# Performance work log

Hardware: AMD Instinct MI355X
Metric: run time of the kernel (lower is better)

The kernel has to match this reference:

```python
import jax, jax.numpy as jnp
import numpy as np

NUM_HEADS = 12
EPS = 1e-5


def _pool_norm(t, w, g, b, thw, stride):
    # t: [B, heads, 1+L, hd]. Depthwise Conv3d pooling on non-cls tokens, then LayerNorm(hd).
    B, Hn, _, hd = t.shape
    cls, body = t[:, :, :1], t[:, :, 1:]
    T, Hs, Ws = thw
    x = body.reshape(B * Hn, T, Hs, Ws, hd).transpose(0, 4, 1, 2, 3)  # [B*heads, hd, T, H, W]
    pad = [(w.shape[2] // 2,) * 2, (w.shape[3] // 2,) * 2, (w.shape[4] // 2,) * 2]
    y = jax.lax.conv_general_dilated(x, w, window_strides=stride, padding=pad,
                                     feature_group_count=hd,
                                     dimension_numbers=('NCDHW', 'OIDHW', 'NCDHW'))
    Tp, Hp, Wp = y.shape[2], y.shape[3], y.shape[4]
    y = y.reshape(B, Hn, hd, Tp * Hp * Wp).transpose(0, 1, 3, 2)  # [B, heads, Lp, hd]
    y = jnp.concatenate([cls, y], axis=2)
    mu = y.mean(-1, keepdims=True)
    var = ((y - mu) ** 2).mean(-1, keepdims=True)
    return (y - mu) * jax.lax.rsqrt(var + EPS) * g + b


def _forward(x, Wq, Wk, Wv, Wproj, b_proj, pq, pk, pv, gq, bq, gk, bk, gv, bv, thw):
    B, N, C = x.shape
    hd = C // NUM_HEADS
    def proj(W):
        return (x @ W.T).reshape(B, N, NUM_HEADS, hd).transpose(0, 2, 1, 3)  # [B, heads, N, hd]
    q = _pool_norm(proj(Wq), pq, gq, bq, thw, (1, 2, 2))
    k = _pool_norm(proj(Wk), pk, gk, bk, thw, (1, 4, 4))
    v = _pool_norm(proj(Wv), pv, gv, bv, thw, (1, 4, 4))
    scale = hd ** -0.5
    attn = jax.nn.softmax(jnp.einsum('bhqd,bhkd->bhqk', q * scale, k), axis=-1)
    o = jnp.einsum('bhqk,bhkd->bhqd', attn, v)
    o = o.transpose(0, 2, 1, 3).reshape(B, o.shape[2], C)
    return o @ Wproj.T + b_proj


def setup_inputs() -> dict:
    key = jax.random.key(0)
    ks = jax.random.split(key, 8)
    B, T, H, W, C = 8, 8, 28, 28, 768
    hd = C // NUM_HEADS
    N = T * H * W + 1  # cls token
    s = lambda k, sh: jax.random.normal(k, sh, jnp.float32) * 0.02
    return {
        'x': jax.random.normal(ks[0], (B, N, C), jnp.float32),
        'Wq': s(ks[1], (C, C)), 'Wk': s(ks[2], (C, C)), 'Wv': s(ks[3], (C, C)),
        'Wproj': s(ks[4], (C, C)), 'b_proj': jnp.zeros((C,), jnp.float32),
        'pool_q_w': s(ks[5], (hd, 1, 3, 3, 3)),
        'pool_k_w': s(ks[6], (hd, 1, 3, 3, 3)),
        'pool_v_w': s(ks[7], (hd, 1, 3, 3, 3)),
        'gq': jnp.ones((hd,), jnp.float32), 'bq': jnp.zeros((hd,), jnp.float32),
        'gk': jnp.ones((hd,), jnp.float32), 'bk': jnp.zeros((hd,), jnp.float32),
        'gv': jnp.ones((hd,), jnp.float32), 'bv': jnp.zeros((hd,), jnp.float32),
        'thw_t': 8, 'thw_h': 28, 'thw_w': 28,
    }


def reference(x, Wq, Wk, Wv, Wproj, b_proj, pool_q_w, pool_k_w, pool_v_w,
              gq, bq, gk, bk, gv, bv, thw_t, thw_h, thw_w):
    return _forward(x, Wq, Wk, Wv, Wproj, b_proj, pool_q_w, pool_k_w, pool_v_w,
                    gq, bq, gk, bk, gv, bv, (thw_t, thw_h, thw_w))
```

## Files before the change

kernel.cpp:

```cpp
#include <hip/hip_runtime.h>

using bf16   = __bf16;
using bf16x4 = __attribute__((ext_vector_type(4))) __bf16;
using bf16x8 = __attribute__((ext_vector_type(8))) __bf16;
using f32x4  = __attribute__((ext_vector_type(4))) float;
using u32x4  = __attribute__((ext_vector_type(4))) unsigned int;

#define MFMA16(a,b,c) __builtin_amdgcn_mfma_f32_16x16x32_bf16((a),(b),(c),0,0,0)

__device__ inline void glds16(const void* g, void* l) {
    __builtin_amdgcn_global_load_lds(
        (__attribute__((address_space(1))) void*)(const_cast<void*>(g)),
        (__attribute__((address_space(3))) void*)(l), 16, 0, 0);
}

__device__ inline int xcd_remap(int bid, int nwg) {
    const int xcd = bid & 7, loc = bid >> 3;
    const int q8 = nwg >> 3, r8 = nwg & 7;
    return (xcd < r8 ? xcd * (q8 + 1) : r8 * (q8 + 1) + (xcd - r8) * q8) + loc;
}

constexpr int CB   = 8;
constexpr int NH   = 12;
constexpr int CC   = 768;
constexpr int HD   = 64;
constexpr int TT   = 8, HH = 28, WW = 28;
constexpr int NTOK = TT*HH*WW + 1;
constexpr int MX   = CB*NTOK;
constexpr int MXP  = 50304;
constexpr int NQ   = 1569, NQP = 1600;
constexpr int NK   = 393,  NKP = 416;
constexpr int MO   = CB*NQ;
constexpr int MOP  = 12672;
constexpr int CTOK = 1 + TT*20*20;
constexpr int MKV  = CB*CTOK;
constexpr int MKVP = 25856;

__global__ __launch_bounds__(256) void cast_f32_bf16(const float* __restrict__ src,
                                                     bf16* __restrict__ dst,
                                                     int nvalid, int ntotal) {
    int i = (blockIdx.x * 256 + threadIdx.x) * 4;
    int stride = gridDim.x * 256 * 4;
    for (; i < ntotal; i += stride) {
        bf16x4 o;
        if (i + 3 < nvalid) {
            f32x4 v = *(const f32x4*)(src + i);
            #pragma unroll
            for (int e = 0; e < 4; ++e) o[e] = (bf16)v[e];
        } else {
            #pragma unroll
            for (int e = 0; e < 4; ++e) {
                int k = i + e;
                o[e] = (bf16)((k < nvalid) ? src[k] : 0.f);
            }
        }
        *(bf16x4*)(dst + i) = o;
    }
}

__global__ __launch_bounds__(256) void cast_w4(const float* __restrict__ w0,
                                               const float* __restrict__ w1,
                                               const float* __restrict__ w2,
                                               const float* __restrict__ w3,
                                               bf16* __restrict__ dst) {
    constexpr int WSZ = 589824;
    int i = (blockIdx.x * 256 + threadIdx.x) * 4;
    if (i >= 4 * WSZ) return;
    const int setn = i / WSZ, j = i % WSZ;
    const float* src = (setn == 0) ? w0 : (setn == 1) ? w1 : (setn == 2) ? w2 : w3;
    f32x4 v = *(const f32x4*)(src + j);
    bf16x4 o;
    #pragma unroll
    for (int e = 0; e < 4; ++e) o[e] = (bf16)v[e];
    *(bf16x4*)(dst + i) = o;
}

__global__ __launch_bounds__(256) void transpose_w3(const float* __restrict__ w0,
                                                    const float* __restrict__ w1,
                                                    const float* __restrict__ w2,
                                                    float* __restrict__ wt) {
    int i = blockIdx.x * 256 + threadIdx.x;
    if (i >= 3 * 1728) return;
    int setn = i / 1728, j = i % 1728;
    const float* src = (setn == 0) ? w0 : (setn == 1) ? w1 : w2;
    int tap = j / 64, c = j % 64;
    wt[i] = src[c * 27 + tap];
}

__global__ void bound_kernel(const float* __restrict__ gq, const float* __restrict__ bq,
                             const float* __restrict__ gk, const float* __restrict__ bk,
                             float* __restrict__ out) {
    const int c = threadIdx.x;
    float mgq = fabsf(gq[c]), sbq = bq[c] * bq[c];
    float mgk = fabsf(gk[c]), sbk = bk[c] * bk[c];
    #pragma unroll
    for (int m = 1; m < 64; m <<= 1) {
        mgq = fmaxf(mgq, __shfl_xor(mgq, m)); sbq += __shfl_xor(sbq, m);
        mgk = fmaxf(mgk, __shfl_xor(mgk, m)); sbk += __shfl_xor(sbk, m);
    }
    if (c == 0) {
        const float Bq = 8.f * mgq + sqrtf(sbq);
        const float Bk = 8.f * mgk + sqrtf(sbk);
        out[0] = 0.125f * Bq * Bk;
    }
}

__global__ __launch_bounds__(512, 2) void gemmU(const bf16* __restrict__ xb,
                                                const bf16* __restrict__ wqkv,
                                                bf16* __restrict__ tmpq,
                                                bf16* __restrict__ tmpkv) {
    extern __shared__ char lds[];
    const int wgid = xcd_remap(blockIdx.x, gridDim.x);

    const int tid = threadIdx.x, lane = tid & 63, w = tid >> 6;
    const int li = lane & 15, lg = lane >> 4;
    const int wr = w >> 2, wc = w & 3;
    const int lr  = lane >> 3;
    const int lsw = ((lane & 7) ^ lr) << 3;

    const bool isQ = wgid < 591;
    int bm, bn, Mv, ldc;
    const bf16* Bb;
    bf16* C;
    if (isQ) { bm = wgid / 3;        bn = wgid % 3;        Mv = MXP;  ldc = 768;
               Bb = wqkv + (size_t)bn * 256 * 768;               C = tmpq; }
    else     { int t = wgid - 591;   bm = t / 6; bn = t % 6; Mv = MKVP; ldc = 1536;
               Bb = wqkv + (size_t)(768 + bn * 256) * 768;       C = tmpkv; }

    const bf16* abase[4];
    const bf16* bbase[4];
    #pragma unroll
    for (int h_ = 0; h_ < 4; ++h_) {
        int gr = bm * 256 + h_ * 64 + w * 8 + lr;
        size_t orig;
        if (isQ) {
            if (gr > MXP - 1) gr = MXP - 1;
            orig = (size_t)gr;
        } else {
            if (gr > MKV - 1) gr = MKV - 1;
            const unsigned b = (unsigned)gr / 3201u;
            const unsigned p = (unsigned)gr % 3201u;
            if (p == 0) orig = (size_t)b * NTOK;
            else {
                const unsigned q  = p - 1;
                const unsigned t2 = q / 400u, rem = q % 400u;
                const unsigned hi = rem / 20u, wi = rem % 20u;
                const int ih = 4 * (int)((hi + 1) / 3) + (int)((hi + 1) % 3) - 1;
                const int iw = 4 * (int)((wi + 1) / 3) + (int)((wi + 1) % 3) - 1;
                orig = (size_t)b * NTOK + 1 + ((size_t)t2 * HH + ih) * WW + iw;
            }
        }
        abase[h_] = xb + orig * 768 + lsw;
        bbase[h_] = Bb + (size_t)(h_ * 64 + w * 8 + lr) * 768 + lsw;
    }

    const int sw_  = (li & 7) << 4;
    const int swc0 = (lg * 16) ^ sw_;
    const int swc1 = (64 | (lg * 16)) ^ sw_;

#define STAGE_AH(Tt, a) do {                                                         \
        char* d_ = lds + ((Tt) & 1) * 65536;                                         \
        glds16(abase[2*(a)]   + (size_t)(Tt) * 64, d_ + ((2*(a))   * 64 + w * 8) * 128); \
        glds16(abase[2*(a)+1] + (size_t)(Tt) * 64, d_ + ((2*(a)+1) * 64 + w * 8) * 128); \
    } while (0)
#define STAGE_BH(Tt, b) do {                                                         \
        char* d_ = lds + ((Tt) & 1) * 65536 + 32768;                                 \
        glds16(bbase[2*(b)]   + (size_t)(Tt) * 64, d_ + ((2*(b))   * 64 + w * 8) * 128); \
        glds16(bbase[2*(b)+1] + (size_t)(Tt) * 64, d_ + ((2*(b)+1) * 64 + w * 8) * 128); \
    } while (0)

    f32x4 acc[8][4] = {};
    bf16x8 aF[4][2], bF0[2][2], bF1[2][2];

#define READ_A(mh)                                                                   \
    _Pragma("unroll") for (int mf = 0; mf < 4; ++mf) {                               \
        const char* p_ = bufA + (size_t)(wr * 128 + (mh) * 64 + mf * 16 + li) * 128; \
        aF[mf][0] = *(const bf16x8*)(p_ + swc0);                                     \
        aF[mf][1] = *(const bf16x8*)(p_ + swc1); }
#define READ_B(nh, BF)                                                               \
    _Pragma("unroll") for (int nf = 0; nf < 2; ++nf) {                               \
        const char* p_ = bufB + (size_t)(wc * 64 + (nh) * 32 + nf * 16 + li) * 128;  \
        BF[nf][0] = *(const bf16x8*)(p_ + swc0);                                     \
        BF[nf][1] = *(const bf16x8*)(p_ + swc1); }
#define MFMA_PH(mh, nh, BF)                                                          \
    _Pragma("unroll") for (int mf = 0; mf < 4; ++mf)                                 \
    _Pragma("unroll") for (int nf = 0; nf < 2; ++nf) {                               \
        acc[(mh)*4+mf][(nh)*2+nf] = MFMA16(aF[mf][0], BF[nf][0], acc[(mh)*4+mf][(nh)*2+nf]); \
        acc[(mh)*4+mf][(nh)*2+nf] = MFMA16(aF[mf][1], BF[nf][1], acc[(mh)*4+mf][(nh)*2+nf]); }

    STAGE_BH(0, 0); STAGE_BH(0, 1); STAGE_AH(0, 0); STAGE_AH(0, 1);
    STAGE_BH(1, 0); STAGE_BH(1, 1); STAGE_AH(1, 0);
    asm volatile("s_waitcnt vmcnt(6)" ::: "memory");
    __builtin_amdgcn_s_barrier();

    #pragma unroll
    for (int k = 0; k < 12; ++k) {
        const char* bufA = lds + (k & 1) * 65536;
        const char* bufB = bufA + 32768;
        READ_A(0); READ_B(0, bF0);
        if (k < 11) STAGE_AH(k + 1, 1);
        __builtin_amdgcn_s_barrier();
        asm volatile("s_waitcnt lgkmcnt(0)" ::: "memory");
        __builtin_amdgcn_s_setprio(1);
        MFMA_PH(0, 0, bF0);
        __builtin_amdgcn_s_setprio(0);
        __builtin_amdgcn_s_barrier();
        READ_B(1, bF1);
        __builtin_amdgcn_s_barrier();
        asm volatile("s_waitcnt lgkmcnt(0)" ::: "memory");
        __builtin_amdgcn_s_setprio(1);
        MFMA_PH(0, 1, bF1);
        __builtin_amdgcn_s_setprio(0);
        __builtin_amdgcn_s_barrier();
        READ_A(1);
        if (k < 10) { STAGE_BH(k + 2, 0); STAGE_BH(k + 2, 1); }
        __builtin_amdgcn_s_barrier();
        asm volatile("s_waitcnt lgkmcnt(0)" ::: "memory");
        __builtin_amdgcn_s_setprio(1);
        MFMA_PH(1, 0, bF0);
        __builtin_amdgcn_s_setprio(0);
        __builtin_amdgcn_s_barrier();
        if (k < 10) STAGE_AH(k + 2, 0);
        __builtin_amdgcn_s_barrier();
        __builtin_amdgcn_s_setprio(1);
        MFMA_PH(1, 1, bF1);
        __builtin_amdgcn_s_setprio(0);
        if (k < 10)       asm volatile("s_waitcnt vmcnt(6)" ::: "memory");
        else if (k == 10) asm volatile("s_waitcnt vmcnt(0)" ::: "memory");
        __builtin_amdgcn_s_barrier();
    }
#undef STAGE_AH
#undef STAGE_BH
#undef READ_A
#undef READ_B
#undef MFMA_PH

    #pragma unroll
    for (int mf = 0; mf < 8; ++mf) {
        const int row0 = bm * 256 + wr * 128 + mf * 16 + lg * 4;
        #pragma unroll
        for (int nf = 0; nf < 4; ++nf) {
            const int col = bn * 256 + wc * 64 + nf * 16 + li;
            #pragma unroll
            for (int r = 0; r < 4; ++r) {
                const int row = row0 + r;
                if (row < Mv)
                    C[(size_t)row * ldc + col] = (bf16)acc[mf][nf][r];
            }
        }
    }
}

__global__ __launch_bounds__(512, 2) void gemmF(const bf16* __restrict__ A,
                                                const bf16* __restrict__ Bw,
                                                float* __restrict__ Cptr,
                                                const float* __restrict__ bias,
                                                int nbn, int Mvalid, int Aclamp) {
    extern __shared__ char lds[];
    const int wgid = xcd_remap(blockIdx.x, gridDim.x);
    const int bm = wgid / nbn, bn = wgid % nbn;

    const int tid = threadIdx.x, lane = tid & 63, w = tid >> 6;
    const int li = lane & 15, lg = lane >> 4;
    const int wr = w >> 2, wc = w & 3;
    const int lr  = lane >> 3;
    const int lsw = ((lane & 7) ^ lr) << 3;
    const bf16* Agp = A  + (size_t)bm * 256 * 768;
    const bf16* Bgp = Bw + (size_t)bn * 128 * 768;
    const int clampA = Aclamp - bm * 256;

    const int sw_  = (li & 7) << 4;
    const int swc0 = (lg * 16) ^ sw_;
    const int swc1 = (64 | (lg * 16)) ^ sw_;

#define STAGE_T(Tt, buf) do {                                                        \
        char* d_ = lds + (buf) * 49152;                                              \
        _Pragma("unroll")                                                            \
        for (int h_ = 0; h_ < 4; ++h_) {                                             \
            const int r0_ = h_ * 64 + w * 8;                                         \
            int gr_ = r0_ + lr; if (gr_ >= clampA) gr_ = clampA - 1;                 \
            glds16(Agp + (size_t)gr_ * 768 + (Tt) * 64 + lsw, d_ + r0_ * 128);       \
        }                                                                            \
        _Pragma("unroll")                                                            \
        for (int h_ = 0; h_ < 2; ++h_) {                                             \
            const int r0_ = h_ * 64 + w * 8;                                         \
            glds16(Bgp + (size_t)(r0_ + lr) * 768 + (Tt) * 64 + lsw,                 \
                   d_ + 32768 + r0_ * 128);                                          \
        } } while (0)

    f32x4 acc[8][2] = {};
    bf16x8 aF[8], bF[2];

#define READ_K(sw)                                                                   \
    _Pragma("unroll") for (int mf = 0; mf < 8; ++mf)                                 \
        aF[mf] = *(const bf16x8*)(bufA + (size_t)(wr * 128 + mf * 16 + li) * 128 + (sw)); \
    _Pragma("unroll") for (int nf = 0; nf < 2; ++nf)                                 \
        bF[nf] = *(const bf16x8*)(bufB + (size_t)(wc * 32 + nf * 16 + li) * 128 + (sw));

#define MFMA_K()                                                                     \
    _Pragma("unroll") for (int mf = 0; mf < 8; ++mf)                                 \
    _Pragma("unroll") for (int nf = 0; nf < 2; ++nf)                                 \
        acc[mf][nf] = MFMA16(aF[mf], bF[nf], acc[mf][nf]);

    STAGE_T(0, 0);
    STAGE_T(1, 1);
    asm volatile("s_waitcnt vmcnt(6)" ::: "memory");
    __builtin_amdgcn_s_barrier();
    __builtin_amdgcn_sched_barrier(0);

    #pragma unroll
    for (int T = 0; T < 12; ++T) {
        const char* bufA = lds + (T & 1) * 49152;
        const char* bufB = bufA + 32768;
        if (T >= 1 && T < 11) STAGE_T(T + 1, (T + 1) & 1);
        READ_K(swc0);
        __builtin_amdgcn_s_setprio(1);
        MFMA_K();
        __builtin_amdgcn_s_setprio(0);
        READ_K(swc1);
        __builtin_amdgcn_s_setprio(1);
        MFMA_K();
        __builtin_amdgcn_s_setprio(0);
        asm volatile("s_waitcnt lgkmcnt(0)" ::: "memory");
        if (T < 11) asm volatile("s_waitcnt vmcnt(0)" ::: "memory");
        __builtin_amdgcn_s_barrier();
        __builtin_amdgcn_sched_barrier(0);
    }
#undef STAGE_T
#undef READ_K
#undef MFMA_K

    #pragma unroll
    for (int mf = 0; mf < 8; ++mf) {
        const int row0 = bm * 256 + wr * 128 + mf * 16 + lg * 4;
        #pragma unroll
        for (int nf = 0; nf < 2; ++nf) {
            const int col = bn * 128 + wc * 32 + nf * 16 + li;
            #pragma unroll
            for (int r = 0; r < 4; ++r) {
                const int row = row0 + r;
                if (row < Mvalid)
                    Cptr[(size_t)row * 768 + col] = acc[mf][nf][r] + bias[col];
            }
        }
    }
}

template<int S, int OH, int OW, int CH, int NP, int NPpad, int SRCSTRIDE, bool COMPACT>
__global__ __launch_bounds__(256) void pool_norm2(const bf16* __restrict__ P,
                                                  const float* __restrict__ wt,
                                                  const float* __restrict__ gamma,
                                                  const float* __restrict__ beta,
                                                  bf16* __restrict__ outp,
                                                  float outScale) {
    constexpr int TASKS = TT * OH * CH + 1;
    const int w = threadIdx.x >> 6, lane = threadIdx.x & 63;
    const int gw = xcd_remap(blockIdx.x, gridDim.x) * 4 + w;
    const int bh = gw / TASKS, task = gw % TASKS;
    const int b = bh / NH, head = bh % NH;
    const int owg = lane >> 3, cg = lane & 7, c = cg * 8;
    const size_t rowbase = COMPACT ? (size_t)b * CTOK : (size_t)b * NTOK;
    const size_t pbase = rowbase * SRCSTRIDE + head * HD + c;

    if (task == TASKS - 1) {
        if (owg == 0) {
            bf16x8 v = *(const bf16x8*)(P + pbase);
            float a[8];
            #pragma unroll
            for (int e = 0; e < 8; ++e) a[e] = (float)v[e];
            float s = 0;
            #pragma unroll
            for (int e = 0; e < 8; ++e) s += a[e];
            s += __shfl_xor(s, 1); s += __shfl_xor(s, 2); s += __shfl_xor(s, 4);
            const float mu = s * 0.015625f;
            float v2 = 0;
            #pragma unroll
            for (int e = 0; e < 8; ++e) { float d = a[e] - mu; v2 += d * d; }
            v2 += __shfl_xor(v2, 1); v2 += __shfl_xor(v2, 2); v2 += __shfl_xor(v2, 4);
            const float rs = rsqrtf(v2 * 0.015625f + 1e-5f);
            f32x4 g0 = *(const f32x4*)(gamma + c), g1 = *(const f32x4*)(gamma + c + 4);
            f32x4 b0 = *(const f32x4*)(beta + c),  b1 = *(const f32x4*)(beta + c + 4);
            bf16x8 o;
            #pragma unroll
            for (int e = 0; e < 4; ++e) {
                o[e]     = (bf16)(((a[e]     - mu) * rs * g0[e] + b0[e]) * outScale);
                o[4 + e] = (bf16)(((a[4 + e] - mu) * rs * g1[e] + b1[e]) * outScale);
            }
            *(bf16x8*)(outp + ((size_t)bh * NPpad) * HD + c) = o;
        } else {
            bf16x8 z = {};
            for (int p = NP + owg - 1; p < NPpad; p += 7)
                *(bf16x8*)(outp + ((size_t)bh * NPpad + p) * HD + c) = z;
        }
        return;
    }

    const int t  = task / (OH * CH);
    const int r2 = task % (OH * CH);
    const int oh = r2 / CH;
    const int ow = (r2 % CH) * 8 + owg;
    const bool active = (ow < OW);

    float acc[8] = {0, 0, 0, 0, 0, 0, 0, 0};
    #pragma unroll
    for (int dt = 0; dt < 3; ++dt) {
        const int it = t + dt - 1;
        if (it < 0 || it >= TT) continue;
        #pragma unroll
        for (int dh = 0; dh < 3; ++dh) {
            int rowh;
            if constexpr (COMPACT) {
                const int hi = 3 * oh + dh - 1;
                if (hi < 0) continue;
                rowh = 1 + it * 400 + hi * 20;
            } else {
                const int ih = oh * S + dh - 1;
                if (ih < 0 || ih >= HH) continue;
                rowh = 1 + (it * HH + ih) * WW;
            }
            #pragma unroll
            for (int dw = 0; dw < 3; ++dw) {
                int rowoff;
                bool ok;
                if constexpr (COMPACT) {
                    const int wi = 3 * ow + dw - 1;
                    ok = active && (wi >= 0);
                    rowoff = rowh + wi;
                } else {
                    const int iw = ow * S + dw - 1;
                    ok = active && (iw >= 0);
                    rowoff = rowh + iw;
                }
                if (ok) {
                    bf16x8 v = *(const bf16x8*)(P + pbase + (size_t)rowoff * SRCSTRIDE);
                    const float* wp = wt + ((dt * 3 + dh) * 3 + dw) * 64 + c;
                    f32x4 w0 = *(const f32x4*)wp, w1 = *(const f32x4*)(wp + 4);
                    #pragma unroll
                    for (int e = 0; e < 4; ++e) {
                        acc[e]     += w0[e] * (float)v[e];
                        acc[4 + e] += w1[e] * (float)v[4 + e];
                    }
                }
            }
        }
    }
    float s = 0;
    #pragma unroll
    for (int e = 0; e < 8; ++e) s += acc[e];
    s += __shfl_xor(s, 1); s += __shfl_xor(s, 2); s += __shfl_xor(s, 4);
    const float mu = s * 0.015625f;
    float v2 = 0;
    #pragma unroll
    for (int e = 0; e < 8; ++e) { float d = acc[e] - mu; v2 += d * d; }
    v2 += __shfl_xor(v2, 1); v2 += __shfl_xor(v2, 2); v2 += __shfl_xor(v2, 4);
    const float rs = rsqrtf(v2 * 0.015625f + 1e-5f);
    if (active) {
        f32x4 g0 = *(const f32x4*)(gamma + c), g1 = *(const f32x4*)(gamma + c + 4);
        f32x4 b0 = *(const f32x4*)(beta + c),  b1 = *(const f32x4*)(beta + c + 4);
        bf16x8 o;
        #pragma unroll
        for (int e = 0; e < 4; ++e) {
            o[e]     = (bf16)(((acc[e]     - mu) * rs * g0[e] + b0[e]) * outScale);
            o[4 + e] = (bf16)(((acc[4 + e] - mu) * rs * g1[e] + b1[e]) * outScale);
        }
        const int p = 1 + (t * OH + oh) * OW + ow;
        *(bf16x8*)(outp + ((size_t)bh * NPpad + p) * HD + c) = o;
    }
}

__global__ __launch_bounds__(256) void attn_kernel(const bf16* __restrict__ qn,
                                                   const bf16* __restrict__ kn,
                                                   const bf16* __restrict__ vn,
                                                   bf16* __restrict__ ob,
                                                   const float* __restrict__ Mptr) {
    __shared__ bf16 Kl[2][32][72];
    __shared__ bf16 Vt[2][64][40];
    __shared__ bf16 Pl[4][16][40];

    const int tid = threadIdx.x, l = tid & 63, w = tid >> 6;
    const int li = l & 15, lg = l >> 4;
    const int wgid = xcd_remap(blockIdx.x, gridDim.x);
    const int bh = wgid / 25;
    const int b = bh / NH, head = bh % NH;
    const int qbase = (wgid % 25) * 64 + w * 16;
    const float M = Mptr[0];

    const bf16* qp = qn + ((size_t)bh * NQP + qbase + li) * HD + lg * 8;
    const bf16x8 aq0 = *(const bf16x8*)qp;
    const bf16x8 aq1 = *(const bf16x8*)(qp + 32);

    const int srow = tid >> 3, scol = (tid & 7) * 8;
    const int sj = tid & 31, sd8 = tid >> 5;
    const bf16* kbase = kn + (size_t)bh * NKP * HD;
    const bf16* vbase = vn + (size_t)bh * NKP * HD;

    u32x4 kv = *(const u32x4*)(kbase + srow * HD + scol);
    u32x4 vv = *(const u32x4*)(vbase + sj * HD + sd8 * 8);
    *(u32x4*)&Kl[0][srow][scol] = kv;
    {
        bf16x8 t = __builtin_bit_cast(bf16x8, vv);
        #pragma unroll
        for (int e = 0; e < 8; ++e) Vt[0][sd8 * 8 + e][sj] = t[e];
    }

    f32x4 oacc[4] = {};
    float lpart[4] = {0.f, 0.f, 0.f, 0.f};

    for (int kt = 0; kt < 13; ++kt) {
        const int cur = kt & 1;
        if (kt < 12) {
            kv = *(const u32x4*)(kbase + (kt + 1) * 32 * HD + srow * HD + scol);
            vv = *(const u32x4*)(vbase + (kt + 1) * 32 * HD + sj * HD + sd8 * 8);
        }
        __syncthreads();

        f32x4 c0 = {}, c1 = {};
        const bf16x8 b00 = *(const bf16x8*)&Kl[cur][li][lg * 8];
        const bf16x8 b01 = *(const bf16x8*)&Kl[cur][li][32 + lg * 8];
        const bf16x8 b10 = *(const bf16x8*)&Kl[cur][16 + li][lg * 8];
        const bf16x8 b11 = *(const bf16x8*)&Kl[cur][16 + li][32 + lg * 8];
        __builtin_amdgcn_s_setprio(1);
        c0 = MFMA16(aq0, b00, c0); c0 = MFMA16(aq1, b01, c0);
        c1 = MFMA16(aq0, b10, c1); c1 = MFMA16(aq1, b11, c1);
        __builtin_amdgcn_s_setprio(0);

        float p0[4], p1[4];
        #pragma unroll
        for (int r = 0; r < 4; ++r) {
            p0[r] = __expf(c0[r] - M);
            p1[r] = __expf(c1[r] - M);
        }
        if (kt == 12) {
            const bool m0 = (384 + li) >= NK;
            #pragma unroll
            for (int r = 0; r < 4; ++r) { if (m0) p0[r] = 0.f; p1[r] = 0.f; }
        }
        #pragma unroll
        for (int r = 0; r < 4; ++r) {
            lpart[r] += p0[r] + p1[r];
            Pl[w][lg * 4 + r][li]      = (bf16)p0[r];
            Pl[w][lg * 4 + r][16 + li] = (bf16)p1[r];
        }
        const bf16x8 ap = *(const bf16x8*)&Pl[w][li][lg * 8];
        __builtin_amdgcn_s_setprio(1);
        #pragma unroll
        for (int dg = 0; dg < 4; ++dg) {
            const bf16x8 bv = *(const bf16x8*)&Vt[cur][dg * 16 + li][lg * 8];
            oacc[dg] = MFMA16(ap, bv, oacc[dg]);
        }
        __builtin_amdgcn_s_setprio(0);

        if (kt < 12) {
            const int nxt = cur ^ 1;
            *(u32x4*)&Kl[nxt][srow][scol] = kv;
            bf16x8 t = __builtin_bit_cast(bf16x8, vv);
            #pragma unroll
            for (int e = 0; e < 8; ++e) Vt[nxt][sd8 * 8 + e][sj] = t[e];
        }
    }
    #pragma unroll
    for (int r = 0; r < 4; ++r) {
        float lsum = lpart[r];
        lsum += __shfl_xor(lsum, 1);
        lsum += __shfl_xor(lsum, 2);
        lsum += __shfl_xor(lsum, 4);
        lsum += __shfl_xor(lsum, 8);
        const int q = qbase + lg * 4 + r;
        if (q < NQ) {
            const float inv = 1.f / lsum;
            const size_t off = ((size_t)(b * NQ + q)) * CC + head * HD;
            #pragma unroll
            for (int dg = 0; dg < 4; ++dg)
                ob[off + dg * 16 + li] = (bf16)(oacc[dg][r] * inv);
        }
    }
}

extern "C" void kernel_launch(void* const* d_in, const int* in_sizes, int n_in,
                              void* d_out, int out_size, void* d_ws, size_t ws_size,
                              hipStream_t stream) {
    const float* x     = (const float*)d_in[0];
    const float* Wq    = (const float*)d_in[1];
    const float* Wk    = (const float*)d_in[2];
    const float* Wv    = (const float*)d_in[3];
    const float* Wproj = (const float*)d_in[4];
    const float* bproj = (const float*)d_in[5];
    const float* pqw   = (const float*)d_in[6];
    const float* pkw   = (const float*)d_in[7];
    const float* pvw   = (const float*)d_in[8];
    const float* gq    = (const float*)d_in[9];
    const float* bq    = (const float*)d_in[10];
    const float* gk    = (const float*)d_in[11];
    const float* bk    = (const float*)d_in[12];
    const float* gv    = (const float*)d_in[13];
    const float* bv    = (const float*)d_in[14];

    if (ws_size < 364000000ULL) return;
    char* ws = (char*)d_ws;
    bf16* xb    = (bf16*)(ws);
    bf16* wqkv  = (bf16*)(ws + 77266944);
    bf16* wpb   = (bf16*)(ws + 80805888);
    bf16* tmpq  = (bf16*)(ws + 81985536);
    bf16* tmpkv = (bf16*)(ws + 159252480);
    bf16* qn    = (bf16*)(ws + 238682112);
    bf16* kn    = (bf16*)(ws + 258342912);
    bf16* vnb   = (bf16*)(ws + 263454720);
    bf16* ob    = (bf16*)(ws + 268566528);
    float* wt   = (float*)(ws + 288030720);
    float* Mb   = (float*)(ws + 288051456);

    (void)hipFuncSetAttribute((const void*)gemmU,
                              hipFuncAttributeMaxDynamicSharedMemorySize, 131072);
    (void)hipFuncSetAttribute((const void*)gemmF,
                              hipFuncAttributeMaxDynamicSharedMemorySize, 98304);

    transpose_w3<<<21, 256, 0, stream>>>(pqw, pkw, pvw, wt);
    bound_kernel<<<1, 64, 0, stream>>>(gq, bq, gk, bk, Mb);
    cast_f32_bf16<<<4096, 256, 0, stream>>>(x, xb, MX * CC, MXP * CC);
    cast_w4<<<2304, 256, 0, stream>>>(Wq, Wk, Wv, Wproj, wqkv);

    gemmU<<<1197, 512, 131072, stream>>>(xb, wqkv, tmpq, tmpkv);

    pool_norm2<2, 14, 14, 2, NQ, NQP, 768,  false><<<5400, 256, 0, stream>>>(tmpq,        wt,        gq, bq, qn,  0.125f);
    pool_norm2<4, 7, 7, 1, NK, NKP, 1536, true ><<<1368, 256, 0, stream>>>(tmpkv,       wt + 1728, gk, bk, kn,  1.0f);
    pool_norm2<4, 7, 7, 1, NK, NKP, 1536, true ><<<1368, 256, 0, stream>>>(tmpkv + 768, wt + 3456, gv, bv, vnb, 1.0f);

    attn_kernel<<<2400, 256, 0, stream>>>(qn, kn, vnb, ob, Mb);

    gemmF<<<50 * 6, 512, 98304, stream>>>(ob, wpb, (float*)d_out, bproj, 6, MO, MOP);
}
```

Baseline: 349.6 us.

## Stage Q pooling input slabs in LDS and merge prep and KV pooling launches

The three small prep kernels (weight cast, pool-weight transpose, bound computation) become one launch. Q pooling now runs per (batch, output row, head) block. Each block stages the needed input rows for all time steps in LDS, so overlapping conv taps read shared memory instead of global memory. K and V pooling, plus the Q cls-token and padding work, are merged into one kernel, which cuts launch count. The cost is about 100KB of LDS per Q block, which limits occupancy, and a larger LDS staging phase behind a barrier.

```diff
diff --git a/kernel.cpp b/kernel.cpp
--- a/kernel.cpp
+++ b/kernel.cpp
@@ -58,50 +58,47 @@
     }
 }
 
-__global__ __launch_bounds__(256) void cast_w4(const float* __restrict__ w0,
-                                               const float* __restrict__ w1,
-                                               const float* __restrict__ w2,
-                                               const float* __restrict__ w3,
-                                               bf16* __restrict__ dst) {
+__global__ __launch_bounds__(256) void prep(const float* __restrict__ Wq, const float* __restrict__ Wk,
+                                            const float* __restrict__ Wv, const float* __restrict__ Wp,
+                                            const float* __restrict__ pqw, const float* __restrict__ pkw,
+                                            const float* __restrict__ pvw,
+                                            const float* __restrict__ gq, const float* __restrict__ bq,
+                                            const float* __restrict__ gk, const float* __restrict__ bk,
+                                            bf16* __restrict__ wdst, float* __restrict__ wt,
+                                            float* __restrict__ Mb) {
     constexpr int WSZ = 589824;
-    int i = (blockIdx.x * 256 + threadIdx.x) * 4;
-    if (i >= 4 * WSZ) return;
-    const int setn = i / WSZ, j = i % WSZ;
-    const float* src = (setn == 0) ? w0 : (setn == 1) ? w1 : (setn == 2) ? w2 : w3;
-    f32x4 v = *(const f32x4*)(src + j);
-    bf16x4 o;
-    #pragma unroll
-    for (int e = 0; e < 4; ++e) o[e] = (bf16)v[e];
-    *(bf16x4*)(dst + i) = o;
-}
-
-__global__ __launch_bounds__(256) void transpose_w3(const float* __restrict__ w0,
-                                                    const float* __restrict__ w1,
-                                                    const float* __restrict__ w2,
-                                                    float* __restrict__ wt) {
-    int i = blockIdx.x * 256 + threadIdx.x;
-    if (i >= 3 * 1728) return;
-    int setn = i / 1728, j = i % 1728;
-    const float* src = (setn == 0) ? w0 : (setn == 1) ? w1 : w2;
-    int tap = j / 64, c = j % 64;
-    wt[i] = src[c * 27 + tap];
-}
-
-__global__ void bound_kernel(const float* __restrict__ gq, const float* __restrict__ bq,
-                             const float* __restrict__ gk, const float* __restrict__ bk,
-                             float* __restrict__ out) {
-    const int c = threadIdx.x;
-    float mgq = fabsf(gq[c]), sbq = bq[c] * bq[c];
-    float mgk = fabsf(gk[c]), sbk = bk[c] * bk[c];
-    #pragma unroll
-    for (int m = 1; m < 64; m <<= 1) {
-        mgq = fmaxf(mgq, __shfl_xor(mgq, m)); sbq += __shfl_xor(sbq, m);
-        mgk = fmaxf(mgk, __shfl_xor(mgk, m)); sbk += __shfl_xor(sbk, m);
-    }
-    if (c == 0) {
-        const float Bq = 8.f * mgq + sqrtf(sbq);
-        const float Bk = 8.f * mgk + sqrtf(sbk);
-        out[0] = 0.125f * Bq * Bk;
+    const int bid = blockIdx.x, tid = threadIdx.x;
+    if (bid < 2304) {
+        int i = (bid * 256 + tid) * 4;
+        const int setn = i / WSZ, j = i % WSZ;
+        const float* src = (setn == 0) ? Wq : (setn == 1) ? Wk : (setn == 2) ? Wv : Wp;
+        f32x4 v = *(const f32x4*)(src + j);
+        bf16x4 o;
+        #pragma unroll
+        for (int e = 0; e < 4; ++e) o[e] = (bf16)v[e];
+        *(bf16x4*)(wdst + i) = o;
+    } else if (bid < 2325) {
+        int i = (bid - 2304) * 256 + tid;
+        if (i < 3 * 1728) {
+            int setn = i / 1728, j = i % 1728;
+            const float* src = (setn == 0) ? pqw : (setn == 1) ? pkw : pvw;
+            int tap = j / 64, c = j % 64;
+            wt[i] = src[c * 27 + tap];
+        }
+    } else if (tid < 64) {
+        const int c = tid;
+        float mgq = fabsf(gq[c]), sbq = bq[c] * bq[c];
+        float mgk = fabsf(gk[c]), sbk = bk[c] * bk[c];
+        #pragma unroll
+        for (int m = 1; m < 64; m <<= 1) {
+            mgq = fmaxf(mgq, __shfl_xor(mgq, m)); sbq += __shfl_xor(sbq, m);
+            mgk = fmaxf(mgk, __shfl_xor(mgk, m)); sbk += __shfl_xor(sbk, m);
+        }
+        if (c == 0) {
+            const float Bq = 8.f * mgq + sqrtf(sbq);
+            const float Bk = 8.f * mgk + sqrtf(sbk);
+            Mb[0] = 0.125f * Bq * Bk;
+        }
     }
 }
 
@@ -346,94 +343,62 @@
     }
 }
 
-template<int S, int OH, int OW, int CH, int NP, int NPpad, int SRCSTRIDE, bool COMPACT>
-__global__ __launch_bounds__(256) void pool_norm2(const bf16* __restrict__ P,
-                                                  const float* __restrict__ wt,
-                                                  const float* __restrict__ gamma,
-                                                  const float* __restrict__ beta,
-                                                  bf16* __restrict__ outp,
-                                                  float outScale) {
-    constexpr int TASKS = TT * OH * CH + 1;
-    const int w = threadIdx.x >> 6, lane = threadIdx.x & 63;
-    const int gw = xcd_remap(blockIdx.x, gridDim.x) * 4 + w;
-    const int bh = gw / TASKS, task = gw % TASKS;
-    const int b = bh / NH, head = bh % NH;
-    const int owg = lane >> 3, cg = lane & 7, c = cg * 8;
-    const size_t rowbase = COMPACT ? (size_t)b * CTOK : (size_t)b * NTOK;
-    const size_t pbase = rowbase * SRCSTRIDE + head * HD + c;
-
-    if (task == TASKS - 1) {
-        if (owg == 0) {
-            bf16x8 v = *(const bf16x8*)(P + pbase);
-            float a[8];
-            #pragma unroll
-            for (int e = 0; e < 8; ++e) a[e] = (float)v[e];
-            float s = 0;
-            #pragma unroll
-            for (int e = 0; e < 8; ++e) s += a[e];
-            s += __shfl_xor(s, 1); s += __shfl_xor(s, 2); s += __shfl_xor(s, 4);
-            const float mu = s * 0.015625f;
-            float v2 = 0;
-            #pragma unroll
-            for (int e = 0; e < 8; ++e) { float d = a[e] - mu; v2 += d * d; }
-            v2 += __shfl_xor(v2, 1); v2 += __shfl_xor(v2, 2); v2 += __shfl_xor(v2, 4);
-            const float rs = rsqrtf(v2 * 0.015625f + 1e-5f);
-            f32x4 g0 = *(const f32x4*)(gamma + c), g1 = *(const f32x4*)(gamma + c + 4);
-            f32x4 b0 = *(const f32x4*)(beta + c),  b1 = *(const f32x4*)(beta + c + 4);
-            bf16x8 o;
-            #pragma unroll
-            for (int e = 0; e < 4; ++e) {
-                o[e]     = (bf16)(((a[e]     - mu) * rs * g0[e] + b0[e]) * outScale);
-                o[4 + e] = (bf16)(((a[4 + e] - mu) * rs * g1[e] + b1[e]) * outScale);
-            }
-            *(bf16x8*)(outp + ((size_t)bh * NPpad) * HD + c) = o;
-        } else {
-            bf16x8 z = {};
-            for (int p = NP + owg - 1; p < NPpad; p += 7)
-                *(bf16x8*)(outp + ((size_t)bh * NPpad + p) * HD + c) = z;
-        }
-        return;
-    }
-
-    const int t  = task / (OH * CH);
-    const int r2 = task % (OH * CH);
-    const int oh = r2 / CH;
-    const int ow = (r2 % CH) * 8 + owg;
-    const bool active = (ow < OW);
-
-    float acc[8] = {0, 0, 0, 0, 0, 0, 0, 0};
-    #pragma unroll
-    for (int dt = 0; dt < 3; ++dt) {
-        const int it = t + dt - 1;
-        if (it < 0 || it >= TT) continue;
-        #pragma unroll
-        for (int dh = 0; dh < 3; ++dh) {
-            int rowh;
-            if constexpr (COMPACT) {
-                const int hi = 3 * oh + dh - 1;
-                if (hi < 0) continue;
-                rowh = 1 + it * 400 + hi * 20;
-            } else {
-                const int ih = oh * S + dh - 1;
-                if (ih < 0 || ih >= HH) continue;
-                rowh = 1 + (it * HH + ih) * WW;
-            }
-            #pragma unroll
-            for (int dw = 0; dw < 3; ++dw) {
-                int rowoff;
-                bool ok;
-                if constexpr (COMPACT) {
-                    const int wi = 3 * ow + dw - 1;
-                    ok = active && (wi >= 0);
-                    rowoff = rowh + wi;
-                } else {
-                    const int iw = ow * S + dw - 1;
-                    ok = active && (iw >= 0);
-                    rowoff = rowh + iw;
-                }
-                if (ok) {
-                    bf16x8 v = *(const bf16x8*)(P + pbase + (size_t)rowoff * SRCSTRIDE);
-                    const float* wp = wt + ((dt * 3 + dh) * 3 + dw) * 64 + c;
+__global__ __launch_bounds__(256) void pool_q_slab(const bf16* __restrict__ tmpq,
+                                                   const float* __restrict__ wt,
+                                                   const float* __restrict__ gamma,
+                                                   const float* __restrict__ beta,
+                                                   bf16* __restrict__ qn) {
+    extern __shared__ char smem[];
+    bf16*  slab = (bf16*)smem;
+    float* wl   = (float*)(smem + 96768);
+    const int bid = blockIdx.x;
+    const int head = bid % 12;
+    int r = bid / 12;
+    const int oh = r % 14;
+    const int b  = r / 14;
+    const int tid = threadIdx.x;
+
+    for (int i = tid; i < 27 * 64; i += 256) wl[i] = wt[i];
+
+    const size_t gbase = ((size_t)b * NTOK + 1) * 768 + head * 64;
+    #pragma unroll
+    for (int dh = 0; dh < 3; ++dh) {
+        const int ih = 2 * oh + dh - 1;
+        if (ih < 0 || ih >= 28) continue;
+        #pragma unroll
+        for (int pass = 0; pass < 7; ++pass) {
+            const int c  = pass * 256 + tid;
+            const int it = c / 224;
+            const int rem = c % 224;
+            const int iw = rem >> 3, cg8 = rem & 7;
+            u32x4 v = *(const u32x4*)(tmpq + gbase + (size_t)((it * 28 + ih) * 28 + iw) * 768 + cg8 * 8);
+            *(u32x4*)&slab[((it * 3 + dh) * 28 + iw) * 72 + cg8 * 8] = v;
+        }
+    }
+    __syncthreads();
+
+    const int cg = tid & 7;
+    #pragma unroll
+    for (int pass = 0; pass < 4; ++pass) {
+        const int item = pass * 32 + (tid >> 3);
+        const bool ok = (item < 112);
+        const int tL = ok ? item / 14 : 0;
+        const int ow = ok ? item % 14 : 0;
+        float acc[8] = {};
+        #pragma unroll
+        for (int dt = 0; dt < 3; ++dt) {
+            const int it = tL + dt - 1;
+            if (it < 0 || it >= 8) continue;
+            #pragma unroll
+            for (int dh = 0; dh < 3; ++dh) {
+                const int ih = 2 * oh + dh - 1;
+                if (ih < 0 || ih >= 28) continue;
+                #pragma unroll
+                for (int dw = 0; dw < 3; ++dw) {
+                    const int iw = 2 * ow + dw - 1;
+                    if (iw < 0 || iw >= 28) continue;
+                    bf16x8 v = *(const bf16x8*)&slab[((it * 3 + dh) * 28 + iw) * 72 + cg * 8];
+                    const float* wp = wl + ((dt * 3 + dh) * 3 + dw) * 64 + cg * 8;
                     f32x4 w0 = *(const f32x4*)wp, w1 = *(const f32x4*)(wp + 4);
                     #pragma unroll
                     for (int e = 0; e < 4; ++e) {
@@ -443,6 +408,156 @@
                 }
             }
         }
+        float s = 0;
+        #pragma unroll
+        for (int e = 0; e < 8; ++e) s += acc[e];
+        s += __shfl_xor(s, 1); s += __shfl_xor(s, 2); s += __shfl_xor(s, 4);
+        const float mu = s * 0.015625f;
+        float v2 = 0;
+        #pragma unroll
+        for (int e = 0; e < 8; ++e) { float d = acc[e] - mu; v2 += d * d; }
+        v2 += __shfl_xor(v2, 1); v2 += __shfl_xor(v2, 2); v2 += __shfl_xor(v2, 4);
+        const float rs = rsqrtf(v2 * 0.015625f + 1e-5f);
+        if (ok) {
+            const int c0 = cg * 8;
+            f32x4 g0 = *(const f32x4*)(gamma + c0), g1 = *(const f32x4*)(gamma + c0 + 4);
+            f32x4 b0 = *(const f32x4*)(beta + c0),  b1 = *(const f32x4*)(beta + c0 + 4);
+            bf16x8 o;
+            #pragma unroll
+            for (int e = 0; e < 4; ++e) {
+                o[e]     = (bf16)(((acc[e]     - mu) * rs * g0[e] + b0[e]) * 0.125f);
+                o[4 + e] = (bf16)(((acc[4 + e] - mu) * rs * g1[e] + b1[e]) * 0.125f);
+            }
+            const int p = 1 + (tL * 14 + oh) * 14 + ow;
+            *(bf16x8*)(qn + ((size_t)(b * 12 + head) * NQP + p) * HD + c0) = o;
+        }
+    }
+}
+
+__global__ __launch_bounds__(256) void pool_kv(const bf16* __restrict__ tmpkv,
+                                               const bf16* __restrict__ tmpq,
+                                               const float* __restrict__ wt,
+                                               const float* __restrict__ gk, const float* __restrict__ bk,
+                                               const float* __restrict__ gv, const float* __restrict__ bv,
+                                               const float* __restrict__ gq, const float* __restrict__ bq,
+                                               bf16* __restrict__ kn, bf16* __restrict__ vnb,
+                                               bf16* __restrict__ qn) {
+    const int w = threadIdx.x >> 6, lane = threadIdx.x & 63;
+    const int gw = xcd_remap(blockIdx.x, gridDim.x) * 4 + w;
+    const int owg = lane >> 3, cg = lane & 7, c = cg * 8;
+
+    if (gw >= 10944) {
+        const int bh = gw - 10944;
+        if (bh >= 96) return;
+        const int b = bh / NH, head = bh % NH;
+        if (owg == 0) {
+            const bf16* src = tmpq + ((size_t)b * NTOK) * CC + head * HD + c;
+            bf16x8 v = *(const bf16x8*)src;
+            float a[8];
+            #pragma unroll
+            for (int e = 0; e < 8; ++e) a[e] = (float)v[e];
+            float s = 0;
+            #pragma unroll
+            for (int e = 0; e < 8; ++e) s += a[e];
+            s += __shfl_xor(s, 1); s += __shfl_xor(s, 2); s += __shfl_xor(s, 4);
+            const float mu = s * 0.015625f;
+            float v2 = 0;
+            #pragma unroll
+            for (int e = 0; e < 8; ++e) { float d = a[e] - mu; v2 += d * d; }
+            v2 += __shfl_xor(v2, 1); v2 += __shfl_xor(v2, 2); v2 += __shfl_xor(v2, 4);
+            const float rs = rsqrtf(v2 * 0.015625f + 1e-5f);
+            f32x4 g0 = *(const f32x4*)(gq + c), g1 = *(const f32x4*)(gq + c + 4);
+            f32x4 b0 = *(const f32x4*)(bq + c), b1 = *(const f32x4*)(bq + c + 4);
+            bf16x8 o;
+            #pragma unroll
+            for (int e = 0; e < 4; ++e) {
+                o[e]     = (bf16)(((a[e]     - mu) * rs * g0[e] + b0[e]) * 0.125f);
+                o[4 + e] = (bf16)(((a[4 + e] - mu) * rs * g1[e] + b1[e]) * 0.125f);
+            }
+            *(bf16x8*)(qn + ((size_t)bh * NQP) * HD + c) = o;
+        } else {
+            bf16x8 z = {};
+            for (int p = NQ + owg - 1; p < NQP; p += 7)
+                *(bf16x8*)(qn + ((size_t)bh * NQP + p) * HD + c) = z;
+        }
+        return;
+    }
+
+    const int set = gw / 5472;
+    const int gw2 = gw % 5472;
+    constexpr int TASKS = TT * 7 + 1;
+    const int bh = gw2 / TASKS, task = gw2 % TASKS;
+    const int b = bh / NH, head = bh % NH;
+    const bf16* P = tmpkv + set * 768;
+    const float* wtp = wt + 1728 + set * 1728;
+    const float* gamma = set ? gv : gk;
+    const float* beta  = set ? bv : bk;
+    bf16* outp = set ? vnb : kn;
+    const size_t pbase = (size_t)b * CTOK * 1536 + head * HD + c;
+
+    if (task == TASKS - 1) {
+        if (owg == 0) {
+            bf16x8 v = *(const bf16x8*)(P + pbase);
+            float a[8];
+            #pragma unroll
+            for (int e = 0; e < 8; ++e) a[e] = (float)v[e];
+            float s = 0;
+            #pragma unroll
+            for (int e = 0; e < 8; ++e) s += a[e];
+            s += __shfl_xor(s, 1); s += __shfl_xor(s, 2); s += __shfl_xor(s, 4);
+            const float mu = s * 0.015625f;
+            float v2 = 0;
+            #pragma unroll
+            for (int e = 0; e < 8; ++e) { float d = a[e] - mu; v2 += d * d; }
+            v2 += __shfl_xor(v2, 1); v2 += __shfl_xor(v2, 2); v2 += __shfl_xor(v2, 4);
+            const float rs = rsqrtf(v2 * 0.015625f + 1e-5f);
+            f32x4 g0 = *(const f32x4*)(gamma + c), g1 = *(const f32x4*)(gamma + c + 4);
+            f32x4 b0 = *(const f32x4*)(beta + c),  b1 = *(const f32x4*)(beta + c + 4);
+            bf16x8 o;
+            #pragma unroll
+            for (int e = 0; e < 4; ++e) {
+                o[e]     = (bf16)((a[e]     - mu) * rs * g0[e] + b0[e]);
+                o[4 + e] = (bf16)((a[4 + e] - mu) * rs * g1[e] + b1[e]);
+            }
+            *(bf16x8*)(outp + ((size_t)bh * NKP) * HD + c) = o;
+        } else {
+            bf16x8 z = {};
+            for (int p = NK + owg - 1; p < NKP; p += 7)
+                *(bf16x8*)(outp + ((size_t)bh * NKP + p) * HD + c) = z;
+        }
+        return;
+    }
+
+    const int t  = task / 7;
+    const int oh = task % 7;
+    const int ow = owg;
+    const bool active = (ow < 7);
+
+    float acc[8] = {};
+    #pragma unroll
+    for (int dt = 0; dt < 3; ++dt) {
+        const int it = t + dt - 1;
+        if (it < 0 || it >= TT) continue;
+        #pragma unroll
+        for (int dh = 0; dh < 3; ++dh) {
+            const int hi = 3 * oh + dh - 1;
+            if (hi < 0) continue;
+            const int rowh = 1 + it * 400 + hi * 20;
+            #pragma unroll
+            for (int dw = 0; dw < 3; ++dw) {
+                const int wi = 3 * ow + dw - 1;
+                if (active && wi >= 0) {
+                    bf16x8 v = *(const bf16x8*)(P + pbase + (size_t)(rowh + wi) * 1536);
+                    const float* wp = wtp + ((dt * 3 + dh) * 3 + dw) * 64 + c;
+                    f32x4 w0 = *(const f32x4*)wp, w1 = *(const f32x4*)(wp + 4);
+                    #pragma unroll
+                    for (int e = 0; e < 4; ++e) {
+                        acc[e]     += w0[e] * (float)v[e];
+                        acc[4 + e] += w1[e] * (float)v[4 + e];
+                    }
+                }
+            }
+        }
     }
     float s = 0;
     #pragma unroll
@@ -460,11 +575,11 @@
         bf16x8 o;
         #pragma unroll
         for (int e = 0; e < 4; ++e) {
-            o[e]     = (bf16)(((acc[e]     - mu) * rs * g0[e] + b0[e]) * outScale);
-            o[4 + e] = (bf16)(((acc[4 + e] - mu) * rs * g1[e] + b1[e]) * outScale);
-        }
-        const int p = 1 + (t * OH + oh) * OW + ow;
-        *(bf16x8*)(outp + ((size_t)bh * NPpad + p) * HD + c) = o;
+            o[e]     = (bf16)((acc[e]     - mu) * rs * g0[e] + b0[e]);
+            o[4 + e] = (bf16)((acc[4 + e] - mu) * rs * g1[e] + b1[e]);
+        }
+        const int p = 1 + (t * 7 + oh) * 7 + ow;
+        *(bf16x8*)(outp + ((size_t)bh * NKP + p) * HD + c) = o;
     }
 }
 
@@ -613,17 +728,17 @@
                               hipFuncAttributeMaxDynamicSharedMemorySize, 131072);
     (void)hipFuncSetAttribute((const void*)gemmF,
                               hipFuncAttributeMaxDynamicSharedMemorySize, 98304);
-
-    transpose_w3<<<21, 256, 0, stream>>>(pqw, pkw, pvw, wt);
-    bound_kernel<<<1, 64, 0, stream>>>(gq, bq, gk, bk, Mb);
+    (void)hipFuncSetAttribute((const void*)pool_q_slab,
+                              hipFuncAttributeMaxDynamicSharedMemorySize, 103680);
+
     cast_f32_bf16<<<4096, 256, 0, stream>>>(x, xb, MX * CC, MXP * CC);
-    cast_w4<<<2304, 256, 0, stream>>>(Wq, Wk, Wv, Wproj, wqkv);
+    prep<<<2326, 256, 0, stream>>>(Wq, Wk, Wv, Wproj, pqw, pkw, pvw,
+                                   gq, bq, gk, bk, wqkv, wt, Mb);
 
     gemmU<<<1197, 512, 131072, stream>>>(xb, wqkv, tmpq, tmpkv);
 
-    pool_norm2<2, 14, 14, 2, NQ, NQP, 768,  false><<<5400, 256, 0, stream>>>(tmpq,        wt,        gq, bq, qn,  0.125f);
-    pool_norm2<4, 7, 7, 1, NK, NKP, 1536, true ><<<1368, 256, 0, stream>>>(tmpkv,       wt + 1728, gk, bk, kn,  1.0f);
-    pool_norm2<4, 7, 7, 1, NK, NKP, 1536, true ><<<1368, 256, 0, stream>>>(tmpkv + 768, wt + 3456, gv, bv, vnb, 1.0f);
+    pool_q_slab<<<1344, 256, 103680, stream>>>(tmpq, wt, gq, bq, qn);
+    pool_kv<<<2760, 256, 0, stream>>>(tmpkv, tmpq, wt, gk, bk, gv, bv, gq, bq, kn, vnb, qn);
 
     attn_kernel<<<2400, 256, 0, stream>>>(qn, kn, vnb, ob, Mb);
 
```

Measured after the change: 373.4 us. 6.8% more time.
